# Performance work log

Measured on AMD Instinct MI355X. Metric: run time of the kernel, lower is better.

Reference implementation:

```python
import jax, jax.numpy as jnp
import numpy as np

DIM = 512
HEADS = 8
DIM_HEAD = 64
INNER = HEADS * DIM_HEAD  # 512
TOPK_FRAC = 0.7
SCALE = DIM_HEAD ** -0.5


def setup_inputs() -> dict:
    key = jax.random.key(0)
    k1, k2, k3, k4 = jax.random.split(key, 4)
    B, N = 4, 1024
    x = jax.random.normal(k1, (B, N, DIM), dtype=jnp.float32)
    # nn.Linear(dim, inner*3, bias=False): weight [3*inner, dim]; store transposed for x @ W
    w_qkv = jax.random.normal(k2, (DIM, 3 * INNER), dtype=jnp.float32) * (DIM ** -0.5)
    # to_out Linear(inner, dim) with bias
    w_out = jax.random.normal(k3, (INNER, DIM), dtype=jnp.float32) * (INNER ** -0.5)
    b_out = jax.random.normal(k4, (DIM,), dtype=jnp.float32) * 0.01
    return {"x": x, "w_qkv": w_qkv, "w_out": w_out, "b_out": b_out}


def reference(x, w_qkv, w_out, b_out):
    B, N, _ = x.shape
    H, D = HEADS, DIM_HEAD
    qkv = x @ w_qkv  # [B, N, 3*INNER]
    q, k, v = jnp.split(qkv, 3, axis=-1)
    # 'b n (h d) -> b h n d'
    reshape = lambda t: t.reshape(B, N, H, D).transpose(0, 2, 1, 3)
    q, k, v = reshape(q), reshape(k), reshape(v)
    dots = jnp.einsum('bhid,bhjd->bhij', q, k) * SCALE  # [B, H, N, N]
    # per-row top-k masking (kNN attention)
    kk = int(N * TOPK_FRAC)
    _, idx = jax.lax.top_k(dots, kk)  # [B, H, N, kk]
    bi = jnp.arange(B)[:, None, None, None]
    hi = jnp.arange(H)[None, :, None, None]
    ii = jnp.arange(N)[None, None, :, None]
    mask = jnp.zeros_like(dots).at[bi, hi, ii, idx].set(1.0)
    dots = jnp.where(mask > 0, dots, jnp.float32(-jnp.inf))
    attn = jax.nn.softmax(dots, axis=-1)
    out = jnp.einsum('bhij,bhjd->bhid', attn, v)  # [B, H, N, D]
    out = out.transpose(0, 2, 1, 3).reshape(B, N, H * D)  # 'b h n d -> b n (h d)'
    return out @ w_out + b_out
```

## Files before the change

### kernel.cpp

```cpp
#include <hip/hip_runtime.h>
#include <cstddef>

#define B_      4
#define N_      1024
#define DIM_    512
#define H_      8
#define D_      64
#define INNER_  512
#define TRIPLE_ 1536
#define KK_     716
#define SCALE_  0.125f

typedef short bf16x8 __attribute__((ext_vector_type(8)));
typedef float f32x4  __attribute__((ext_vector_type(4)));
typedef unsigned short ushort_t;
typedef ushort_t us8 __attribute__((ext_vector_type(8)));

__device__ __forceinline__ unsigned short bf16_rne(float f) {
    unsigned u = __float_as_uint(f);
    return (unsigned short)((u + 0x7FFFu + ((u >> 16) & 1u)) >> 16);
}
__device__ __forceinline__ float bf16_f(unsigned short s) {
    return __uint_as_float((unsigned)s << 16);
}
__device__ __forceinline__ unsigned f2key(float f) {
    unsigned u = __float_as_uint(f);
    return u ^ ((u & 0x80000000u) ? 0xFFFFFFFFu : 0x80000000u);
}
__device__ __forceinline__ float key2f(unsigned k) {
    unsigned u = (k & 0x80000000u) ? (k ^ 0x80000000u) : ~k;
    return __uint_as_float(u);
}
__device__ __forceinline__ int wave_count(int lc) {
    int c = __popcll(__ballot(lc & 1));
    c += __popcll(__ballot(lc & 2)) << 1;
    c += __popcll(__ballot(lc & 4)) << 2;
    c += __popcll(__ballot(lc & 8)) << 3;
    c += __popcll(__ballot(lc & 16)) << 4;
    return c;
}
__device__ __forceinline__ int count_ge(const unsigned* key, unsigned kt) {
    int lc = 0;
#pragma unroll
    for (int m = 0; m < 16; ++m) lc += (key[m] >= kt) ? 1 : 0;
    return wave_count(lc);
}
__device__ __forceinline__ unsigned topk_thresh(const unsigned* key, float mu, float sg) {
    unsigned res = 0u;
    bool found = false;
    float tlo = 0.f, thi = 0.f;
    int   clo = 0,   chi = 0;
    bool  hlo = false, hhi = false;
    float tcur = mu - 0.52189f * sg;
    for (int it = 0; it < 10; ++it) {
        const unsigned kt = f2key(tcur);
        const int c = count_ge(key, kt);
        if (c == KK_) { res = kt; found = true; break; }
        if (c > KK_) { tlo = tcur; clo = c; hlo = true; }
        else         { thi = tcur; chi = c; hhi = true; }
        float tn;
        if (hlo && hhi) {
            tn = tlo + (thi - tlo) * ((float)(clo - KK_) / (float)(clo - chi));
        } else {
            const float z    = (tcur - mu) / sg;
            const float dens = fmaxf(408.5f * __expf(-0.5f * z * z) / sg, 1.f);
            tn = tcur + (float)(c - KK_) / dens;
        }
        if (hlo && !(tn > tlo)) tn = hhi ? 0.5f * (tlo + thi) : tlo + 0.25f * sg;
        if (hhi && !(tn < thi)) tn = hlo ? 0.5f * (tlo + thi) : thi - 0.25f * sg;
        tcur = tn;
    }
    if (!found) {
        unsigned klo = hlo ? f2key(tlo) : 0u;
        unsigned khi = hhi ? f2key(thi) : 0xFFFFFFFFu;
        while (khi - klo > 1u) {
            const unsigned km = klo + ((khi - klo) >> 1);
            const int c = count_ge(key, km);
            if (c >= KK_) { klo = km; if (c == KK_) break; }
            else khi = km;
        }
        res = klo;
    }
    return res;
}
__device__ __forceinline__ void split8(const float* __restrict__ src,
                                       bf16x8& h8, bf16x8& l8) {
    float4 a = *(const float4*)src;
    float4 b = *(const float4*)(src + 4);
    float v[8] = {a.x, a.y, a.z, a.w, b.x, b.y, b.z, b.w};
#pragma unroll
    for (int i = 0; i < 8; ++i) {
        ushort_t hb = bf16_rne(v[i]);
        h8[i] = (short)hb;
        l8[i] = (short)bf16_rne(v[i] - bf16_f(hb));
    }
}

__global__ __launch_bounds__(256) void conv_wT2(const float* __restrict__ Wq,
                                                const float* __restrict__ Wo,
                                                ushort_t* __restrict__ WqTh,
                                                ushort_t* __restrict__ WqTl,
                                                ushort_t* __restrict__ WoTh,
                                                ushort_t* __restrict__ WoTl) {
    __shared__ float tile[32][33];
    const bool isQ = blockIdx.x < 48;
    const int  nb  = (isQ ? blockIdx.x : blockIdx.x - 48) * 32;
    const int  kb  = blockIdx.y * 32;
    const int  Nn  = isQ ? TRIPLE_ : DIM_;
    const float* W = isQ ? Wq : Wo;
    ushort_t* Th   = isQ ? WqTh : WoTh;
    ushort_t* Tl   = isQ ? WqTl : WoTl;
    const int tx = threadIdx.x & 31, ty = threadIdx.x >> 5;
    for (int yy = ty; yy < 32; yy += 8)
        tile[yy][tx] = W[(size_t)(kb + yy) * Nn + nb + tx];
    __syncthreads();
    for (int yy = ty; yy < 32; yy += 8) {
        float v = tile[tx][yy];
        ushort_t hb = bf16_rne(v);
        size_t idx = (size_t)(nb + yy) * DIM_ + kb + tx;
        Th[idx] = hb;
        Tl[idx] = bf16_rne(v - bf16_f(hb));
    }
}

__global__ __launch_bounds__(256) void gemm_qkv_mfma(
    const float* __restrict__ X,
    const ushort_t* __restrict__ Wh, const ushort_t* __restrict__ Wl,
    ushort_t* __restrict__ Qh, ushort_t* __restrict__ Ql,
    ushort_t* __restrict__ Kh, ushort_t* __restrict__ Kl,
    ushort_t* __restrict__ Vt) {
    __shared__ ushort_t stile[4][4608];
    __shared__ ushort_t BshH[2][2048];
    __shared__ ushort_t BshL[2][2048];
    const int t = threadIdx.x, w = t >> 6, l = t & 63;
    const int ln = l & 15, quad = l >> 4;
    const int n0 = blockIdx.y * 64;
    const int m0 = blockIdx.x * 128 + w * 32;
    f32x4 acc[2][4] = {};
    {
        const size_t xrow0 = (size_t)(m0 + ln) * DIM_;
        const size_t xrow1 = (size_t)(m0 + 16 + ln) * DIM_;
        const int srow = t >> 2;
        const int sk   = (t & 3) << 3;
        const size_t gb = (size_t)(n0 + srow) * DIM_ + sk;
        us8 nh = *(const us8*)&Wh[gb];
        us8 nl = *(const us8*)&Wl[gb];
        *(us8*)&BshH[0][t * 8] = nh;
        *(us8*)&BshL[0][t * 8] = nl;
        int cur = 0;
        for (int k0 = 0; k0 < DIM_; k0 += 32) {
            const bool more = (k0 + 32) < DIM_;
            const size_t gnext = gb + (size_t)(more ? k0 + 32 : 0);
            nh = *(const us8*)&Wh[gnext];
            nl = *(const us8*)&Wl[gnext];
            __syncthreads();
            const int ko = k0 + quad * 8;
            bf16x8 ah0, al0, ah1, al1;
            split8(&X[xrow0 + ko], ah0, al0);
            split8(&X[xrow1 + ko], ah1, al1);
#pragma unroll
            for (int j = 0; j < 4; ++j) {
                const int slot = (((j << 4) + ln) << 5) + (quad << 3);
                bf16x8 bh = *(const bf16x8*)&BshH[cur][slot];
                bf16x8 bl = *(const bf16x8*)&BshL[cur][slot];
                acc[0][j] = __builtin_amdgcn_mfma_f32_16x16x32_bf16(ah0, bh, acc[0][j], 0, 0, 0);
                acc[0][j] = __builtin_amdgcn_mfma_f32_16x16x32_bf16(al0, bh, acc[0][j], 0, 0, 0);
                acc[0][j] = __builtin_amdgcn_mfma_f32_16x16x32_bf16(ah0, bl, acc[0][j], 0, 0, 0);
                acc[1][j] = __builtin_amdgcn_mfma_f32_16x16x32_bf16(ah1, bh, acc[1][j], 0, 0, 0);
                acc[1][j] = __builtin_amdgcn_mfma_f32_16x16x32_bf16(al1, bh, acc[1][j], 0, 0, 0);
                acc[1][j] = __builtin_amdgcn_mfma_f32_16x16x32_bf16(ah1, bl, acc[1][j], 0, 0, 0);
            }
            if (more) {
                *(us8*)&BshH[cur ^ 1][t * 8] = nh;
                *(us8*)&BshL[cur ^ 1][t * 8] = nl;
            }
            cur ^= 1;
        }
    }
    const int sec = n0 >> 9;
    const int h   = (n0 >> 6) & 7;
    ushort_t* tw  = stile[w];
    const int b = m0 >> 10, nnb = m0 & 1023;
    if (sec < 2) {
        ushort_t* Hp = sec ? Kh : Qh;
        ushort_t* Lp = sec ? Kl : Ql;
#pragma unroll
        for (int i = 0; i < 2; ++i)
#pragma unroll
            for (int j = 0; j < 4; ++j)
#pragma unroll
                for (int g = 0; g < 4; ++g) {
                    const float v = acc[i][j][g];
                    const ushort_t hb = bf16_rne(v);
                    const ushort_t lb = bf16_rne(v - bf16_f(hb));
                    const int tok = i * 16 + quad * 4 + g;
                    const int d   = j * 16 + ln;
                    tw[tok * 72 + d]        = hb;
                    tw[2304 + tok * 72 + d] = lb;
                }
        __syncthreads();
        const size_t rowbase = ((size_t)(b * 8 + h) * 1024 + nnb) * 64;
        const int dd = (l & 7) * 8;
#pragma unroll
        for (int s = 0; s < 4; ++s) {
            const int tl = s * 8 + (l >> 3);
            const size_t off = rowbase + (size_t)tl * 64 + dd;
            *(us8*)&Hp[off] = *(const us8*)&tw[tl * 72 + dd];
            *(us8*)&Lp[off] = *(const us8*)&tw[2304 + tl * 72 + dd];
        }
    } else {
#pragma unroll
        for (int i = 0; i < 2; ++i)
#pragma unroll
            for (int j = 0; j < 4; ++j)
#pragma unroll
                for (int g = 0; g < 4; ++g)
                    tw[(j * 16 + ln) * 40 + i * 16 + quad * 4 + g] = bf16_rne(acc[i][j][g]);
        __syncthreads();
        const size_t vbase = (size_t)(b * 8 + h) * 65536 + nnb;
#pragma unroll
        for (int p = 0; p < 2; ++p) {
            const int d = (p << 5) + (l >> 1);
            const int c = (l & 1) << 4;
            ushort_t* dst = &Vt[vbase + (size_t)d * 1024 + c];
            *(us8*)dst       = *(const us8*)&tw[d * 40 + c];
            *(us8*)(dst + 8) = *(const us8*)&tw[d * 40 + c + 8];
        }
    }
}

__global__ __launch_bounds__(256) void gemm_out_mfma(
    const ushort_t* __restrict__ Ah, const ushort_t* __restrict__ Al,
    const ushort_t* __restrict__ Wh, const ushort_t* __restrict__ Wl,
    const float* __restrict__ bias, float* __restrict__ C) {
    __shared__ ushort_t BshH[2][2048];
    __shared__ ushort_t BshL[2][2048];
    const int t = threadIdx.x, w = t >> 6, l = t & 63;
    const int ln = l & 15, quad = l >> 4;
    const int n0 = blockIdx.y * 64;
    const int m0 = blockIdx.x * 128 + w * 32;
    f32x4 acc[2][4] = {};
    {
        const size_t arow0 = (size_t)(m0 + ln) * INNER_;
        const size_t arow1 = (size_t)(m0 + 16 + ln) * INNER_;
        const int srow = t >> 2;
        const int sk   = (t & 3) << 3;
        const size_t gb = (size_t)(n0 + srow) * INNER_ + sk;
        us8 nh = *(const us8*)&Wh[gb];
        us8 nl = *(const us8*)&Wl[gb];
        *(us8*)&BshH[0][t * 8] = nh;
        *(us8*)&BshL[0][t * 8] = nl;
        int cur = 0;
        for (int k0 = 0; k0 < INNER_; k0 += 32) {
            const bool more = (k0 + 32) < INNER_;
            const size_t gnext = gb + (size_t)(more ? k0 + 32 : 0);
            nh = *(const us8*)&Wh[gnext];
            nl = *(const us8*)&Wl[gnext];
            __syncthreads();
            const int ko = k0 + quad * 8;
            bf16x8 ah0 = *(const bf16x8*)&Ah[arow0 + ko];
            bf16x8 al0 = *(const bf16x8*)&Al[arow0 + ko];
            bf16x8 ah1 = *(const bf16x8*)&Ah[arow1 + ko];
            bf16x8 al1 = *(const bf16x8*)&Al[arow1 + ko];
#pragma unroll
            for (int j = 0; j < 4; ++j) {
                const int slot = (((j << 4) + ln) << 5) + (quad << 3);
                bf16x8 bh = *(const bf16x8*)&BshH[cur][slot];
                bf16x8 bl = *(const bf16x8*)&BshL[cur][slot];
                acc[0][j] = __builtin_amdgcn_mfma_f32_16x16x32_bf16(ah0, bh, acc[0][j], 0, 0, 0);
                acc[0][j] = __builtin_amdgcn_mfma_f32_16x16x32_bf16(al0, bh, acc[0][j], 0, 0, 0);
                acc[0][j] = __builtin_amdgcn_mfma_f32_16x16x32_bf16(ah0, bl, acc[0][j], 0, 0, 0);
                acc[1][j] = __builtin_amdgcn_mfma_f32_16x16x32_bf16(ah1, bh, acc[1][j], 0, 0, 0);
                acc[1][j] = __builtin_amdgcn_mfma_f32_16x16x32_bf16(al1, bh, acc[1][j], 0, 0, 0);
                acc[1][j] = __builtin_amdgcn_mfma_f32_16x16x32_bf16(ah1, bl, acc[1][j], 0, 0, 0);
            }
            if (more) {
                *(us8*)&BshH[cur ^ 1][t * 8] = nh;
                *(us8*)&BshL[cur ^ 1][t * 8] = nl;
            }
            cur ^= 1;
        }
    }
#pragma unroll
    for (int i = 0; i < 2; ++i)
#pragma unroll
        for (int j = 0; j < 4; ++j) {
            const int col = n0 + j * 16 + ln;
            const float bb = bias[col];
#pragma unroll
            for (int g = 0; g < 4; ++g) {
                const int token = m0 + i * 16 + quad * 4 + g;
                C[(size_t)token * DIM_ + col] = acc[i][j][g] + bb;
            }
        }
}

__global__ __launch_bounds__(512, 4) void attn_mfma(const ushort_t* __restrict__ Qh,
                                                    const ushort_t* __restrict__ Ql,
                                                    const ushort_t* __restrict__ Kh,
                                                    const ushort_t* __restrict__ Kl,
                                                    const ushort_t* __restrict__ Vt,
                                                    ushort_t* __restrict__ Oh,
                                                    ushort_t* __restrict__ Ol) {
    __shared__ float sdots[16 * 1024];
    __shared__ float spartial[4][16][17];

    const int t    = threadIdx.x;
    const int w    = t >> 6;
    const int l    = t & 63;
    const int ln   = l & 15;
    const int quad = l >> 4;
    const int wg   = blockIdx.x;
    const int bh   = wg & 31;
    const int i0   = (wg >> 5) << 4;

    const size_t bhoff = (size_t)bh << 16;

    const ushort_t* qp  = Qh + bhoff + (size_t)(i0 + ln) * 64 + (quad << 3);
    const ushort_t* qlp = Ql + bhoff + (size_t)(i0 + ln) * 64 + (quad << 3);
    bf16x8 qh0 = *(const bf16x8*)qp;
    bf16x8 qh1 = *(const bf16x8*)(qp + 32);
    bf16x8 ql0 = *(const bf16x8*)qlp;
    bf16x8 ql1 = *(const bf16x8*)(qlp + 32);

    for (int tt = 0; tt < 8; ++tt) {
        const int j0 = ((w << 3) + tt) << 4;
        const ushort_t* kp  = Kh + bhoff + (size_t)(j0 + ln) * 64 + (quad << 3);
        const ushort_t* klp = Kl + bhoff + (size_t)(j0 + ln) * 64 + (quad << 3);
        bf16x8 kh0 = *(const bf16x8*)kp;
        bf16x8 kh1 = *(const bf16x8*)(kp + 32);
        bf16x8 kl0 = *(const bf16x8*)klp;
        bf16x8 kl1 = *(const bf16x8*)(klp + 32);
        f32x4 acc = {0.f, 0.f, 0.f, 0.f};
        acc = __builtin_amdgcn_mfma_f32_16x16x32_bf16(qh0, kh0, acc, 0, 0, 0);
        acc = __builtin_amdgcn_mfma_f32_16x16x32_bf16(qh1, kh1, acc, 0, 0, 0);
        acc = __builtin_amdgcn_mfma_f32_16x16x32_bf16(qh0, kl0, acc, 0, 0, 0);
        acc = __builtin_amdgcn_mfma_f32_16x16x32_bf16(qh1, kl1, acc, 0, 0, 0);
        acc = __builtin_amdgcn_mfma_f32_16x16x32_bf16(ql0, kh0, acc, 0, 0, 0);
        acc = __builtin_amdgcn_mfma_f32_16x16x32_bf16(ql1, kh1, acc, 0, 0, 0);
#pragma unroll
        for (int g = 0; g < 4; ++g) {
            const int row = (quad << 2) + g;
            sdots[(row << 10) + ((j0 + ln) ^ ((row & 7) << 2))] = acc[g] * SCALE_;
        }
    }
    __syncthreads();

    ushort_t* sP = (ushort_t*)sdots;
    {
        const int r0 = w << 1, r1 = r0 | 1;
        const int swz0 = (r0 & 7) << 2, swz1 = (r1 & 7) << 2;
        const float* s0 = &sdots[r0 << 10];
        const float* s1 = &sdots[r1 << 10];
        unsigned key0[16], key1[16];
        float sa0 = 0.f, sb0 = 0.f, sa1 = 0.f, sb1 = 0.f;
#pragma unroll
        for (int m = 0; m < 4; ++m) {
            f32x4 kv0 = *(const f32x4*)&s0[((l << 2) + (m << 8)) ^ swz0];
            f32x4 kv1 = *(const f32x4*)&s1[((l << 2) + (m << 8)) ^ swz1];
#pragma unroll
            for (int i = 0; i < 4; ++i) {
                key0[(m << 2) + i] = f2key(kv0[i]);
                key1[(m << 2) + i] = f2key(kv1[i]);
                sa0 += kv0[i];
                sb0 += kv0[i] * kv0[i];
                sa1 += kv1[i];
                sb1 += kv1[i] * kv1[i];
            }
        }
#pragma unroll
        for (int off = 32; off; off >>= 1) {
            sa0 += __shfl_xor(sa0, off, 64);
            sb0 += __shfl_xor(sb0, off, 64);
            sa1 += __shfl_xor(sa1, off, 64);
            sb1 += __shfl_xor(sb1, off, 64);
        }
        const float mu0 = sa0 * (1.0f / 1024.f);
        const float sg0 = sqrtf(fmaxf(sb0 * (1.0f / 1024.f) - mu0 * mu0, 1e-20f));
        const float mu1 = sa1 * (1.0f / 1024.f);
        const float sg1 = sqrtf(fmaxf(sb1 * (1.0f / 1024.f) - mu1 * mu1, 1e-20f));

        const unsigned res0 = topk_thresh(key0, mu0, sg0);
        const unsigned res1 = topk_thresh(key1, mu1, sg1);

        const float thr0 = key2f(res0), thr1 = key2f(res1);
        float pv0[16], pv1[16];
        float ls0 = 0.f, ls1 = 0.f;
#pragma unroll
        for (int m = 0; m < 16; ++m) {
            float p0 = (key0[m] >= res0) ? __expf(key2f(key0[m]) - thr0) : 0.f;
            float p1 = (key1[m] >= res1) ? __expf(key2f(key1[m]) - thr1) : 0.f;
            pv0[m] = p0;
            pv1[m] = p1;
            ls0 += p0;
            ls1 += p1;
        }
#pragma unroll
        for (int off = 32; off; off >>= 1) {
            ls0 += __shfl_xor(ls0, off, 64);
            ls1 += __shfl_xor(ls1, off, 64);
        }
        const float inv0 = 1.f / ls0, inv1 = 1.f / ls1;
#pragma unroll
        for (int m = 0; m < 4; ++m) {
            const int g0 = ((l >> 1) + (m << 5)) ^ (r0 & 7);
            const int g1 = ((l >> 1) + (m << 5)) ^ (r1 & 7);
            ushort4 pk0 = make_ushort4(bf16_rne(pv0[(m << 2) + 0] * inv0),
                                       bf16_rne(pv0[(m << 2) + 1] * inv0),
                                       bf16_rne(pv0[(m << 2) + 2] * inv0),
                                       bf16_rne(pv0[(m << 2) + 3] * inv0));
            ushort4 pk1 = make_ushort4(bf16_rne(pv1[(m << 2) + 0] * inv1),
                                       bf16_rne(pv1[(m << 2) + 1] * inv1),
                                       bf16_rne(pv1[(m << 2) + 2] * inv1),
                                       bf16_rne(pv1[(m << 2) + 3] * inv1));
            *(ushort4*)&sP[(r0 << 11) + (g0 << 3) + ((l & 1) << 2)] = pk0;
            *(ushort4*)&sP[(r1 << 11) + (g1 << 3) + ((l & 1) << 2)] = pk1;
        }
    }
    __syncthreads();

    const int dblk  = w & 3;
    const int jbase = (w & 4) << 7;
    f32x4 oacc = {0.f, 0.f, 0.f, 0.f};
    const ushort_t* vp =
        Vt + bhoff + (size_t)((dblk << 4) + ln) * 1024 + (quad << 3) + jbase;
    const int prow = ln << 11;
    const int rsw  = ln & 7;
#pragma unroll
    for (int j0 = 0; j0 < 512; j0 += 32) {
        const int g = ((jbase + j0) >> 3) + quad;
        bf16x8 af = *(const bf16x8*)&sP[prow + ((g ^ rsw) << 3)];
        bf16x8 bv = *(const bf16x8*)(vp + j0);
        oacc = __builtin_amdgcn_mfma_f32_16x16x32_bf16(af, bv, oacc, 0, 0, 0);
    }
    if (w & 4) {
#pragma unroll
        for (int g = 0; g < 4; ++g)
            spartial[dblk][(quad << 2) + g][ln] = oacc[g];
    }
    __syncthreads();
    if (!(w & 4)) {
        const int b = bh >> 3, h = bh & 7;
        const size_t obase =
            ((size_t)(b << 10) + i0 + (quad << 2)) * 512 + (h << 6) + (dblk << 4) + ln;
#pragma unroll
        for (int g = 0; g < 4; ++g) {
            const float v = oacc[g] + spartial[dblk][(quad << 2) + g][ln];
            ushort_t hb = bf16_rne(v);
            Oh[obase + (size_t)g * 512] = hb;
            Ol[obase + (size_t)g * 512] = bf16_rne(v - bf16_f(hb));
        }
    }
}

extern "C" void kernel_launch(void* const* d_in, const int* in_sizes, int n_in,
                              void* d_out, int out_size, void* d_ws, size_t ws_size,
                              hipStream_t stream) {
    const float* x     = (const float*)d_in[0];
    const float* w_qkv = (const float*)d_in[1];
    const float* w_out = (const float*)d_in[2];
    const float* b_out = (const float*)d_in[3];
    float*       out   = (float*)d_out;

    const size_t ON  = (size_t)4096 * 512;
    const size_t WQT = (size_t)1536 * 512;
    const size_t WOT = (size_t)512 * 512;
    const size_t QK  = (size_t)32 * 1024 * 64;

    ushort_t* p    = (ushort_t*)d_ws;
    ushort_t* Oh   = p;            p += ON;
    ushort_t* Ol   = p;            p += ON;
    ushort_t* WqTh = p;            p += WQT;
    ushort_t* WqTl = p;            p += WQT;
    ushort_t* WoTh = p;            p += WOT;
    ushort_t* WoTl = p;            p += WOT;
    ushort_t* Qh   = p;            p += QK;
    ushort_t* Ql   = p;            p += QK;
    ushort_t* Kh   = p;            p += QK;
    ushort_t* Kl   = p;            p += QK;
    ushort_t* Vt   = p;            p += QK;

    conv_wT2<<<dim3(64, 16), 256, 0, stream>>>(w_qkv, w_out, WqTh, WqTl, WoTh, WoTl);

    gemm_qkv_mfma<<<dim3(4096 / 128, TRIPLE_ / 64), 256, 0, stream>>>(
        x, WqTh, WqTl, Qh, Ql, Kh, Kl, Vt);

    attn_mfma<<<dim3(B_ * H_ * (N_ / 16)), 512, 0, stream>>>(Qh, Ql, Kh, Kl, Vt, Oh, Ol);

    gemm_out_mfma<<<dim3(4096 / 128, DIM_ / 64), 256, 0, stream>>>(
        Oh, Ol, WoTh, WoTl, b_out, out);
}
```

Baseline: 225.1 us.

## Halve attention LDS score buffer via two-pass QK and interleave dual top-k searches

The attention kernel now computes the 16x1024 score tile in two halves of 512 columns, reusing a 32 KB shared buffer instead of 64 KB. Each half is converted to sort keys and moment sums in registers before the buffer is reused. This is meant to let more workgroups fit per CU. The two per-row top-k threshold searches are also merged into one loop so their wave-wide counts can overlap. The softmax scale is folded into the Q projection epilogue. The cost is an extra barrier and a round of LDS reads, and more live registers across phases.

Result: slower. 231.1 us (+2.7%).

```diff
diff --git a/kernel.cpp b/kernel.cpp
--- a/kernel.cpp
+++ b/kernel.cpp
@@ -45,43 +45,82 @@
     for (int m = 0; m < 16; ++m) lc += (key[m] >= kt) ? 1 : 0;
     return wave_count(lc);
 }
-__device__ __forceinline__ unsigned topk_thresh(const unsigned* key, float mu, float sg) {
-    unsigned res = 0u;
-    bool found = false;
-    float tlo = 0.f, thi = 0.f;
-    int   clo = 0,   chi = 0;
-    bool  hlo = false, hhi = false;
-    float tcur = mu - 0.52189f * sg;
+__device__ __forceinline__ unsigned bisect_exact(const unsigned* key,
+                                                 bool hlo, bool hhi,
+                                                 float tlo, float thi) {
+    unsigned klo = hlo ? f2key(tlo) : 0u;
+    unsigned khi = hhi ? f2key(thi) : 0xFFFFFFFFu;
+    while (khi - klo > 1u) {
+        const unsigned km = klo + ((khi - klo) >> 1);
+        const int c = count_ge(key, km);
+        if (c >= KK_) { klo = km; if (c == KK_) break; }
+        else khi = km;
+    }
+    return klo;
+}
+__device__ __forceinline__ void topk2(const unsigned* key0, const unsigned* key1,
+                                      float mu0, float sg0, float mu1, float sg1,
+                                      unsigned& out0, unsigned& out1) {
+    bool done0 = false, done1 = false;
+    float tlo0 = 0.f, thi0 = 0.f, tlo1 = 0.f, thi1 = 0.f;
+    int   clo0 = 0,   chi0 = 0,   clo1 = 0,   chi1 = 0;
+    bool  hlo0 = false, hhi0 = false, hlo1 = false, hhi1 = false;
+    float t0 = mu0 - 0.52189f * sg0;
+    float t1 = mu1 - 0.52189f * sg1;
+    unsigned res0 = 0u, res1 = 0u;
     for (int it = 0; it < 10; ++it) {
-        const unsigned kt = f2key(tcur);
-        const int c = count_ge(key, kt);
-        if (c == KK_) { res = kt; found = true; break; }
-        if (c > KK_) { tlo = tcur; clo = c; hlo = true; }
-        else         { thi = tcur; chi = c; hhi = true; }
-        float tn;
-        if (hlo && hhi) {
-            tn = tlo + (thi - tlo) * ((float)(clo - KK_) / (float)(clo - chi));
-        } else {
-            const float z    = (tcur - mu) / sg;
-            const float dens = fmaxf(408.5f * __expf(-0.5f * z * z) / sg, 1.f);
-            tn = tcur + (float)(c - KK_) / dens;
-        }
-        if (hlo && !(tn > tlo)) tn = hhi ? 0.5f * (tlo + thi) : tlo + 0.25f * sg;
-        if (hhi && !(tn < thi)) tn = hlo ? 0.5f * (tlo + thi) : thi - 0.25f * sg;
-        tcur = tn;
-    }
-    if (!found) {
-        unsigned klo = hlo ? f2key(tlo) : 0u;
-        unsigned khi = hhi ? f2key(thi) : 0xFFFFFFFFu;
-        while (khi - klo > 1u) {
-            const unsigned km = klo + ((khi - klo) >> 1);
-            const int c = count_ge(key, km);
-            if (c >= KK_) { klo = km; if (c == KK_) break; }
-            else khi = km;
-        }
-        res = klo;
-    }
-    return res;
+        if (done0 & done1) break;
+        const unsigned kt0 = f2key(t0);
+        const unsigned kt1 = f2key(t1);
+        int lc0 = 0, lc1 = 0;
+#pragma unroll
+        for (int m = 0; m < 16; ++m) {
+            lc0 += (key0[m] >= kt0) ? 1 : 0;
+            lc1 += (key1[m] >= kt1) ? 1 : 0;
+        }
+        const int c0 = wave_count(lc0);
+        const int c1 = wave_count(lc1);
+        if (!done0) {
+            if (c0 == KK_) { res0 = kt0; done0 = true; }
+            else {
+                if (c0 > KK_) { tlo0 = t0; clo0 = c0; hlo0 = true; }
+                else          { thi0 = t0; chi0 = c0; hhi0 = true; }
+                float tn;
+                if (hlo0 && hhi0) {
+                    tn = tlo0 + (thi0 - tlo0) * ((float)(clo0 - KK_) / (float)(clo0 - chi0));
+                } else {
+                    const float z    = (t0 - mu0) / sg0;
+                    const float dens = fmaxf(408.5f * __expf(-0.5f * z * z) / sg0, 1.f);
+                    tn = t0 + (float)(c0 - KK_) / dens;
+                }
+                if (hlo0 && !(tn > tlo0)) tn = hhi0 ? 0.5f * (tlo0 + thi0) : tlo0 + 0.25f * sg0;
+                if (hhi0 && !(tn < thi0)) tn = hlo0 ? 0.5f * (tlo0 + thi0) : thi0 - 0.25f * sg0;
+                t0 = tn;
+            }
+        }
+        if (!done1) {
+            if (c1 == KK_) { res1 = kt1; done1 = true; }
+            else {
+                if (c1 > KK_) { tlo1 = t1; clo1 = c1; hlo1 = true; }
+                else          { thi1 = t1; chi1 = c1; hhi1 = true; }
+                float tn;
+                if (hlo1 && hhi1) {
+                    tn = tlo1 + (thi1 - tlo1) * ((float)(clo1 - KK_) / (float)(clo1 - chi1));
+                } else {
+                    const float z    = (t1 - mu1) / sg1;
+                    const float dens = fmaxf(408.5f * __expf(-0.5f * z * z) / sg1, 1.f);
+                    tn = t1 + (float)(c1 - KK_) / dens;
+                }
+                if (hlo1 && !(tn > tlo1)) tn = hhi1 ? 0.5f * (tlo1 + thi1) : tlo1 + 0.25f * sg1;
+                if (hhi1 && !(tn < thi1)) tn = hlo1 ? 0.5f * (tlo1 + thi1) : thi1 - 0.25f * sg1;
+                t1 = tn;
+            }
+        }
+    }
+    if (!done0) res0 = bisect_exact(key0, hlo0, hhi0, tlo0, thi0);
+    if (!done1) res1 = bisect_exact(key1, hlo1, hhi1, tlo1, thi1);
+    out0 = res0;
+    out1 = res1;
 }
 __device__ __forceinline__ void split8(const float* __restrict__ src,
                                        bf16x8& h8, bf16x8& l8) {
@@ -184,13 +223,14 @@
     if (sec < 2) {
         ushort_t* Hp = sec ? Kh : Qh;
         ushort_t* Lp = sec ? Kl : Ql;
+        const float qsc = sec ? 1.0f : SCALE_;
 #pragma unroll
         for (int i = 0; i < 2; ++i)
 #pragma unroll
             for (int j = 0; j < 4; ++j)
 #pragma unroll
                 for (int g = 0; g < 4; ++g) {
-                    const float v = acc[i][j][g];
+                    const float v = acc[i][j][g] * qsc;
                     const ushort_t hb = bf16_rne(v);
                     const ushort_t lb = bf16_rne(v - bf16_f(hb));
                     const int tok = i * 16 + quad * 4 + g;
@@ -302,7 +342,7 @@
                                                     const ushort_t* __restrict__ Vt,
                                                     ushort_t* __restrict__ Oh,
                                                     ushort_t* __restrict__ Ol) {
-    __shared__ float sdots[16 * 1024];
+    __shared__ float sdots[16 * 512];
     __shared__ float spartial[4][16][17];
 
     const int t    = threadIdx.x;
@@ -323,8 +363,17 @@
     bf16x8 ql0 = *(const bf16x8*)qlp;
     bf16x8 ql1 = *(const bf16x8*)(qlp + 32);
 
-    for (int tt = 0; tt < 8; ++tt) {
-        const int j0 = ((w << 3) + tt) << 4;
+    const int r0 = w << 1, r1 = r0 | 1;
+    const int swz0 = (r0 & 7) << 2, swz1 = (r1 & 7) << 2;
+    const float* s0 = &sdots[r0 << 9];
+    const float* s1 = &sdots[r1 << 9];
+
+    unsigned key0[16], key1[16];
+    float sa0 = 0.f, sb0 = 0.f, sa1 = 0.f, sb1 = 0.f;
+
+#pragma unroll
+    for (int tt = 0; tt < 4; ++tt) {
+        const int j0 = (w << 6) + (tt << 4);
         const ushort_t* kp  = Kh + bhoff + (size_t)(j0 + ln) * 64 + (quad << 3);
         const ushort_t* klp = Kl + bhoff + (size_t)(j0 + ln) * 64 + (quad << 3);
         bf16x8 kh0 = *(const bf16x8*)kp;
@@ -341,33 +390,67 @@
 #pragma unroll
         for (int g = 0; g < 4; ++g) {
             const int row = (quad << 2) + g;
-            sdots[(row << 10) + ((j0 + ln) ^ ((row & 7) << 2))] = acc[g] * SCALE_;
+            sdots[(row << 9) + ((j0 + ln) ^ ((row & 7) << 2))] = acc[g];
         }
     }
     __syncthreads();
+#pragma unroll
+    for (int m = 0; m < 2; ++m) {
+        f32x4 kv0 = *(const f32x4*)&s0[((l << 2) + (m << 8)) ^ swz0];
+        f32x4 kv1 = *(const f32x4*)&s1[((l << 2) + (m << 8)) ^ swz1];
+#pragma unroll
+        for (int i = 0; i < 4; ++i) {
+            key0[(m << 2) + i] = f2key(kv0[i]);
+            key1[(m << 2) + i] = f2key(kv1[i]);
+            sa0 += kv0[i];
+            sb0 += kv0[i] * kv0[i];
+            sa1 += kv1[i];
+            sb1 += kv1[i] * kv1[i];
+        }
+    }
+    __syncthreads();
+
+#pragma unroll
+    for (int tt = 0; tt < 4; ++tt) {
+        const int j0 = 512 + (w << 6) + (tt << 4);
+        const ushort_t* kp  = Kh + bhoff + (size_t)(j0 + ln) * 64 + (quad << 3);
+        const ushort_t* klp = Kl + bhoff + (size_t)(j0 + ln) * 64 + (quad << 3);
+        bf16x8 kh0 = *(const bf16x8*)kp;
+        bf16x8 kh1 = *(const bf16x8*)(kp + 32);
+        bf16x8 kl0 = *(const bf16x8*)klp;
+        bf16x8 kl1 = *(const bf16x8*)(klp + 32);
+        f32x4 acc = {0.f, 0.f, 0.f, 0.f};
+        acc = __builtin_amdgcn_mfma_f32_16x16x32_bf16(qh0, kh0, acc, 0, 0, 0);
+        acc = __builtin_amdgcn_mfma_f32_16x16x32_bf16(qh1, kh1, acc, 0, 0, 0);
+        acc = __builtin_amdgcn_mfma_f32_16x16x32_bf16(qh0, kl0, acc, 0, 0, 0);
+        acc = __builtin_amdgcn_mfma_f32_16x16x32_bf16(qh1, kl1, acc, 0, 0, 0);
+        acc = __builtin_amdgcn_mfma_f32_16x16x32_bf16(ql0, kh0, acc, 0, 0, 0);
+        acc = __builtin_amdgcn_mfma_f32_16x16x32_bf16(ql1, kh1, acc, 0, 0, 0);
+#pragma unroll
+        for (int g = 0; g < 4; ++g) {
+            const int row = (quad << 2) + g;
+            const int jl  = (j0 - 512) + ln;
+            sdots[(row << 9) + (jl ^ ((row & 7) << 2))] = acc[g];
+        }
+    }
+    __syncthreads();
+#pragma unroll
+    for (int m = 0; m < 2; ++m) {
+        f32x4 kv0 = *(const f32x4*)&s0[((l << 2) + (m << 8)) ^ swz0];
+        f32x4 kv1 = *(const f32x4*)&s1[((l << 2) + (m << 8)) ^ swz1];
+#pragma unroll
+        for (int i = 0; i < 4; ++i) {
+            key0[8 + (m << 2) + i] = f2key(kv0[i]);
+            key1[8 + (m << 2) + i] = f2key(kv1[i]);
+            sa0 += kv0[i];
+            sb0 += kv0[i] * kv0[i];
+            sa1 += kv1[i];
+            sb1 += kv1[i] * kv1[i];
+        }
+    }
 
     ushort_t* sP = (ushort_t*)sdots;
     {
-        const int r0 = w << 1, r1 = r0 | 1;
-        const int swz0 = (r0 & 7) << 2, swz1 = (r1 & 7) << 2;
-        const float* s0 = &sdots[r0 << 10];
-        const float* s1 = &sdots[r1 << 10];
-        unsigned key0[16], key1[16];
-        float sa0 = 0.f, sb0 = 0.f, sa1 = 0.f, sb1 = 0.f;
-#pragma unroll
-        for (int m = 0; m < 4; ++m) {
-            f32x4 kv0 = *(const f32x4*)&s0[((l << 2) + (m << 8)) ^ swz0];
-            f32x4 kv1 = *(const f32x4*)&s1[((l << 2) + (m << 8)) ^ swz1];
-#pragma unroll
-            for (int i = 0; i < 4; ++i) {
-                key0[(m << 2) + i] = f2key(kv0[i]);
-                key1[(m << 2) + i] = f2key(kv1[i]);
-                sa0 += kv0[i];
-                sb0 += kv0[i] * kv0[i];
-                sa1 += kv1[i];
-                sb1 += kv1[i] * kv1[i];
-            }
-        }
 #pragma unroll
         for (int off = 32; off; off >>= 1) {
             sa0 += __shfl_xor(sa0, off, 64);
@@ -380,8 +463,8 @@
         const float mu1 = sa1 * (1.0f / 1024.f);
         const float sg1 = sqrtf(fmaxf(sb1 * (1.0f / 1024.f) - mu1 * mu1, 1e-20f));
 
-        const unsigned res0 = topk_thresh(key0, mu0, sg0);
-        const unsigned res1 = topk_thresh(key1, mu1, sg1);
+        unsigned res0, res1;
+        topk2(key0, key1, mu0, sg0, mu1, sg1, res0, res1);
 
         const float thr0 = key2f(res0), thr1 = key2f(res1);
         float pv0[16], pv1[16];
@@ -413,8 +496,8 @@
                                        bf16_rne(pv1[(m << 2) + 1] * inv1),
                                        bf16_rne(pv1[(m << 2) + 2] * inv1),
                                        bf16_rne(pv1[(m << 2) + 3] * inv1));
-            *(ushort4*)&sP[(r0 << 11) + (g0 << 3) + ((l & 1) << 2)] = pk0;
-            *(ushort4*)&sP[(r1 << 11) + (g1 << 3) + ((l & 1) << 2)] = pk1;
+            *(ushort4*)&sP[(r0 << 10) + (g0 << 3) + ((l & 1) << 2)] = pk0;
+            *(ushort4*)&sP[(r1 << 10) + (g1 << 3) + ((l & 1) << 2)] = pk1;
         }
     }
     __syncthreads();
@@ -424,7 +507,7 @@
     f32x4 oacc = {0.f, 0.f, 0.f, 0.f};
     const ushort_t* vp =
         Vt + bhoff + (size_t)((dblk << 4) + ln) * 1024 + (quad << 3) + jbase;
-    const int prow = ln << 11;
+    const int prow = ln << 10;
     const int rsw  = ln & 7;
 #pragma unroll
     for (int j0 = 0; j0 < 512; j0 += 32) {
```
